# Optimization experiments

Measured on AMD Instinct MI355X. Metric: run time of the kernel, lower is better.

## Reference

```python
import jax, jax.numpy as jnp
import numpy as np

K = 3
P = 14
INV_SQRT2 = 0.7071067811865476  # db1 (Haar) filter coefficient
EPS = 1e-4


def _pool(x):
    # adaptive_avg_pool2d to (P, P); H, W divisible by P -> uniform mean pooling
    N, C, H, W = x.shape
    return x.reshape(N, C, P, H // P, P, W // P).mean(axis=(3, 5))


def setup_inputs() -> dict:
    key = jax.random.key(0)
    ks = jax.random.split(key, 8)
    N, C, H, W = 64, 3, 224, 224
    D, Cin = 540, 30  # D_clip=D_hidden=540, n_bands*3 = 30
    return {
        "frames": jax.random.normal(ks[0], (N, C, H, W), jnp.float32),
        "t_clip": jax.random.normal(ks[1], (N, D, P, P), jnp.float32),
        "w1": jax.random.normal(ks[2], (D, Cin), jnp.float32) * 0.05,
        "b1": jnp.zeros((D,), jnp.float32),
        "w2": jax.random.normal(ks[3], (D, D), jnp.float32) * 0.05,
        "b2": jnp.zeros((D,), jnp.float32),
        "wg": jax.random.normal(ks[4], (D, 2 * D, 3, 3), jnp.float32) * 0.05,
        "bg": jnp.zeros((D,), jnp.float32),
    }


def reference(frames, t_clip, w1, b1, w2, b2, wg, bg):
    # Batched Haar SWT2 (a trous, periodic), levels 1..K, fully vectorized over
    # (N, C) -- replaces the per-frame/per-channel pywt.swt2 CPU loop.
    a = frames
    bands = []  # per level: HL (cH), LH (cV), HH (cD), each (N, C, H, W)
    for j in range(K):
        d = 2 ** j  # filter dilation at level j+1
        lx = (a + jnp.roll(a, -d, axis=-1)) * INV_SQRT2
        hx = (a - jnp.roll(a, -d, axis=-1)) * INV_SQRT2
        cA = (lx + jnp.roll(lx, -d, axis=-2)) * INV_SQRT2
        cH = (lx - jnp.roll(lx, -d, axis=-2)) * INV_SQRT2
        cV = (hx + jnp.roll(hx, -d, axis=-2)) * INV_SQRT2
        cD = (hx - jnp.roll(hx, -d, axis=-2)) * INV_SQRT2
        bands += [cH, cV, cD]
        a = cA
    # per-(frame, channel) 99th-percentile normalization + pool to (P, P)
    pooled = []
    for b in bands:
        s = jnp.quantile(jnp.abs(b), 0.99, axis=(-2, -1), keepdims=True)
        pooled.append(_pool(b / (s + EPS)))
    # LL band (level K approximation): mean-center then quantile-scale
    mu = a.mean(axis=(-2, -1), keepdims=True)
    s = jnp.quantile(jnp.abs(a - mu), 0.99, axis=(-2, -1), keepdims=True)
    pooled.append(_pool((a - mu) / (s + EPS)))
    e_pix = jnp.concatenate(pooled, axis=1)  # (N, 30, P, P)

    # 1x1 conv -> relu -> 1x1 conv -> tanh
    h = jax.nn.relu(jnp.einsum("ncpq,dc->ndpq", e_pix, w1) + b1[None, :, None, None])
    m = jnp.tanh(jnp.einsum("ncpq,dc->ndpq", h, w2) + b2[None, :, None, None])

    # gated fusion with CLIP patch tokens
    gi = jnp.concatenate([t_clip, m], axis=1)  # (N, 2*D, P, P)
    g = jax.lax.conv_general_dilated(
        gi, wg, (1, 1), "SAME", dimension_numbers=("NCHW", "OIHW", "NCHW")
    ) + bg[None, :, None, None]
    gamma = jax.nn.sigmoid(g)
    return t_clip + gamma * m
```

## Files before the change

kernel.cpp:

```cpp
#include <hip/hip_runtime.h>

typedef unsigned short u16;
typedef unsigned int u32;
typedef __bf16 bf16x8 __attribute__((ext_vector_type(8)));
typedef float f32x4 __attribute__((ext_vector_type(4)));

constexpr int NB = 64, CH3 = 3;
constexpr int PLANES = NB * CH3;
constexpr int PPIX = 224 * 224;
constexpr int PP = 196;
constexpr int NPX = NB * PP;
constexpr int K2 = 576;
constexpr int CIPAD = 1088;
constexpr int KCONV = 9 * CIPAD;
constexpr int BINS = 256;
constexpr int BIN0 = 896;
constexpr int RANK1 = 49674;
constexpr int RANK2 = 49675;

constexpr size_t OFF_HIST = 0;
constexpr size_t SZ_HIST  = (size_t)10 * PLANES * BINS * 4;
constexpr size_t OFF_SUMS = OFF_HIST + SZ_HIST;
constexpr size_t OFF_INVS = OFF_SUMS + 768;
constexpr size_t OFF_BSUM = OFF_INVS + 7680;
constexpr size_t SZ_BSUM  = (size_t)10 * PLANES * PP * 4;
constexpr size_t OFF_EPIX = OFF_BSUM + SZ_BSUM;
constexpr size_t OFF_HBF  = OFF_EPIX + (size_t)NPX * 32 * 4;
constexpr size_t OFF_GIT  = OFF_HBF + (size_t)NPX * K2 * 2;
constexpr size_t SZ_GIT   = (size_t)NB * 256 * CIPAD * 2;
constexpr size_t OFF_WGB  = OFF_GIT + SZ_GIT;
constexpr size_t OFF_W2B  = OFF_WGB + (size_t)640 * KCONV * 2;
constexpr size_t OFF_MARR = OFF_W2B + (size_t)640 * K2 * 2;

__device__ __forceinline__ u16 f2bf(float x) {
  union { float f; u32 u; } c; c.f = x;
  u32 r = c.u + 0x7FFFu + ((c.u >> 16) & 1u);
  return (u16)(r >> 16);
}

__device__ __forceinline__ float wred64(float v) {
  v += __shfl_down(v, 32, 64); v += __shfl_down(v, 16, 64);
  v += __shfl_down(v, 8, 64);  v += __shfl_down(v, 4, 64);
  v += __shfl_down(v, 2, 64);  v += __shfl_down(v, 1, 64);
  return v;
}

__device__ __forceinline__ float gred16(float v) {
  v += __shfl_down(v, 8, 16); v += __shfl_down(v, 4, 16);
  v += __shfl_down(v, 2, 16); v += __shfl_down(v, 1, 16);
  return v;
}

__device__ __forceinline__ int hbin(float v) {
  int b = (int)(__float_as_uint(fabsf(v)) >> 20) - BIN0;
  return min(max(b, 0), BINS - 1);
}

__device__ __forceinline__ void cp16(const void* g, void* l) {
  __builtin_amdgcn_global_load_lds((const __attribute__((address_space(1))) u32*)g,
                                   (__attribute__((address_space(3))) u32*)l, 16, 0, 0);
}

__device__ __forceinline__ float fast_tanh(float x) {
  return 1.f - 2.f / (1.f + __expf(2.f * x));
}
__device__ __forceinline__ float fast_sigmoid(float x) {
  return 1.f / (1.f + __expf(-x));
}

#define BAR_MEM() asm volatile("s_barrier" ::: "memory")

constexpr int RSTRIDE = 10 * 128 + 8;
__global__ __launch_bounds__(256) void swt_fused_kernel(const float* __restrict__ frames,
    float* __restrict__ sums, int* __restrict__ hist, float* __restrict__ bsum)
{
  __shared__ float a1[22 * 224];
  __shared__ float a2[20 * 224];
  __shared__ u32 lh[8 * RSTRIDE];
  __shared__ float csum[14 * 10];
  __shared__ float wsum[4];
  const int t = threadIdx.x;
  const int rb = blockIdx.x, plane = blockIdx.y;
  const float* Pp = frames + (size_t)plane * PPIX;

  for (int i = t; i < 8 * RSTRIDE; i += 256) lh[i] = 0;
  __syncthreads();

  u32* lhr = &lh[(t & 7) * RSTRIDE];
  const int cell0 = (t >> 4) * 10;
  float ps = 0.f;

  if (t < 224) {
    int c2 = t + 1; if (c2 >= 224) c2 -= 224;
    float sH = 0.f, sV = 0.f, sD = 0.f;
    int gr0 = rb * 16; if (gr0 >= 224) gr0 -= 224;
    float q00 = Pp[gr0 * 224 + t], q01 = Pp[gr0 * 224 + c2];
    for (int r = 0; r < 22; ++r) {
      int gr1 = rb * 16 + r + 1; if (gr1 >= 224) gr1 -= 224;
      float p10 = Pp[gr1 * 224 + t], p11 = Pp[gr1 * 224 + c2];
      float sa = q00 + q01, sb = p10 + p11, da = q00 - q01, db = p10 - p11;
      a1[r * 224 + t] = (sa + sb) * 0.5f;
      if (r < 16) {
        float cH = (sa - sb) * 0.5f, cV = (da + db) * 0.5f, cD = (da - db) * 0.5f;
        int bH = hbin(cH), bV = hbin(cV), bD = hbin(cD);
        atomicAdd(&lhr[0 * 128 + (bH >> 1)], 1u << ((bH & 1) * 16));
        atomicAdd(&lhr[1 * 128 + (bV >> 1)], 1u << ((bV & 1) * 16));
        atomicAdd(&lhr[2 * 128 + (bD >> 1)], 1u << ((bD & 1) * 16));
        sH += cH; sV += cV; sD += cD;
        ps += q00;
      }
      q00 = p10; q01 = p11;
    }
    sH = gred16(sH); sV = gred16(sV); sD = gred16(sD);
    if ((t & 15) == 0) { csum[cell0 + 0] = sH; csum[cell0 + 1] = sV; csum[cell0 + 2] = sD; }
  }
  ps = wred64(ps);
  if ((t & 63) == 0) wsum[t >> 6] = ps;
  __syncthreads();
  if (t == 0) atomicAdd(&sums[plane], wsum[0] + wsum[1] + wsum[2] + wsum[3]);

  if (t < 224) {
    int c2 = t + 2; if (c2 >= 224) c2 -= 224;
    float sH = 0.f, sV = 0.f, sD = 0.f;
    for (int r = 0; r < 20; ++r) {
      float p00 = a1[r * 224 + t], p01 = a1[r * 224 + c2];
      float p10 = a1[(r + 2) * 224 + t], p11 = a1[(r + 2) * 224 + c2];
      float sa = p00 + p01, sb = p10 + p11, da = p00 - p01, db = p10 - p11;
      a2[r * 224 + t] = (sa + sb) * 0.5f;
      if (r < 16) {
        float cH = (sa - sb) * 0.5f, cV = (da + db) * 0.5f, cD = (da - db) * 0.5f;
        int bH = hbin(cH), bV = hbin(cV), bD = hbin(cD);
        atomicAdd(&lhr[3 * 128 + (bH >> 1)], 1u << ((bH & 1) * 16));
        atomicAdd(&lhr[4 * 128 + (bV >> 1)], 1u << ((bV & 1) * 16));
        atomicAdd(&lhr[5 * 128 + (bD >> 1)], 1u << ((bD & 1) * 16));
        sH += cH; sV += cV; sD += cD;
      }
    }
    sH = gred16(sH); sV = gred16(sV); sD = gred16(sD);
    if ((t & 15) == 0) { csum[cell0 + 3] = sH; csum[cell0 + 4] = sV; csum[cell0 + 5] = sD; }
  }
  __syncthreads();

  if (t < 224) {
    int c2 = t + 4; if (c2 >= 224) c2 -= 224;
    float sH = 0.f, sV = 0.f, sD = 0.f, sA = 0.f;
    for (int r = 0; r < 16; ++r) {
      float p00 = a2[r * 224 + t], p01 = a2[r * 224 + c2];
      float p10 = a2[(r + 4) * 224 + t], p11 = a2[(r + 4) * 224 + c2];
      float sa = p00 + p01, sb = p10 + p11, da = p00 - p01, db = p10 - p11;
      float cA = (sa + sb) * 0.5f;
      float cH = (sa - sb) * 0.5f, cV = (da + db) * 0.5f, cD = (da - db) * 0.5f;
      int bH = hbin(cH), bV = hbin(cV), bD = hbin(cD), bA = hbin(cA);
      atomicAdd(&lhr[6 * 128 + (bH >> 1)], 1u << ((bH & 1) * 16));
      atomicAdd(&lhr[7 * 128 + (bV >> 1)], 1u << ((bV & 1) * 16));
      atomicAdd(&lhr[8 * 128 + (bD >> 1)], 1u << ((bD & 1) * 16));
      atomicAdd(&lhr[9 * 128 + (bA >> 1)], 1u << ((bA & 1) * 16));
      sH += cH; sV += cV; sD += cD; sA += cA;
    }
    sH = gred16(sH); sV = gred16(sV); sD = gred16(sD); sA = gred16(sA);
    if ((t & 15) == 0) {
      csum[cell0 + 6] = sH; csum[cell0 + 7] = sV; csum[cell0 + 8] = sD; csum[cell0 + 9] = sA;
    }
  }
  __syncthreads();

  for (int i = t; i < 10 * 256; i += 256) {
    int bg = i >> 8, b = i & 255;
    u32 acc = 0;
#pragma unroll
    for (int rp = 0; rp < 8; ++rp)
      acc += (lh[rp * RSTRIDE + bg * 128 + (b >> 1)] >> ((b & 1) * 16)) & 0xFFFFu;
    if (acc) atomicAdd(&hist[((size_t)bg * PLANES + plane) * BINS + b], (int)acc);
  }
  if (t < 140) {
    int cell = t / 10, bg = t - cell * 10;
    bsum[((size_t)bg * PLANES + plane) * PP + rb * 14 + cell] = csum[cell * 10 + bg];
  }
}

__global__ __launch_bounds__(256) void quant_kernel(const int* __restrict__ hist,
    float* __restrict__ invs)
{
  const int g = blockIdx.x;
  __shared__ int cum[BINS];
  __shared__ float vv[2];
  const int t = threadIdx.x;
  const int c = hist[(size_t)g * BINS + t];
  cum[t] = c;
  __syncthreads();
  for (int off = 1; off < BINS; off <<= 1) {
    int y = (t >= off) ? cum[t - off] : 0;
    __syncthreads();
    cum[t] += y;
    __syncthreads();
  }
  int inc = cum[t], prev = inc - c;
#pragma unroll
  for (int k = 0; k < 2; ++k) {
    int rank = k ? RANK2 : RANK1;
    if (prev < rank && rank <= inc) {
      float lo = __uint_as_float((u32)(t + BIN0) << 20);
      float hi = __uint_as_float((u32)(t + BIN0 + 1) << 20);
      float fr = ((float)(rank - prev) - 0.5f) / (float)c;
      fr = fminf(fmaxf(fr, 0.f), 1.f);
      vv[k] = lo + (hi - lo) * fr;
    }
  }
  __syncthreads();
  if (t == 0) {
    float s = 0.75f * vv[0] + 0.25f * vv[1];
    invs[g] = 1.f / (s + 1e-4f);
  }
}

__global__ __launch_bounds__(256) void pack_all_kernel(const float* __restrict__ wg,
    const float* __restrict__ w2, const float* __restrict__ tclip,
    u16* __restrict__ wgb, u16* __restrict__ w2b, u16* __restrict__ git)
{
  __shared__ float sh[9720];
  const int bid = blockIdx.x;
  const int t = threadIdx.x;
  if (bid < 640) {
    const int oc = bid;
    if (oc < 540) {
      for (int i = t; i < 9720; i += 256) sh[i] = wg[(size_t)oc * 9720 + i];
    }
    __syncthreads();
    for (int j = t; j < KCONV; j += 256) {
      int kc = j >> 6, i = j & 63;
      int cib = kc / 9, tap = kc - cib * 9;
      int ci = cib * 64 + i;
      float v = (oc < 540 && ci < 1080) ? sh[ci * 9 + tap] : 0.f;
      wgb[(size_t)oc * KCONV + j] = f2bf(v);
    }
  } else if (bid < 2080) {
    int tid = (bid - 640) * 256 + t;
    int oc = tid / K2, cc = tid - oc * K2;
    float v = (oc < 540 && cc < 540) ? w2[oc * 540 + cc] : 0.f;
    w2b[tid] = f2bf(v);
  } else if (bid < 4169) {
    constexpr int CPB = 136;
    constexpr int CPN = 60 * CPB + 196;
    int tid = (bid - 2080) * 256 + t;
    if (tid >= NB * CPN) return;
    int n = tid / CPN, rem = tid - n * CPN;
    int y, x, c;
    if (rem < 60 * CPB) {
      int bi = rem / CPB; c = rem - bi * CPB;
      if (bi < 16) { y = 0; x = bi; }
      else if (bi < 32) { y = 15; x = bi - 16; }
      else { int i = bi - 32; y = 1 + (i >> 1); x = (i & 1) * 15; }
    } else {
      int q = rem - 60 * CPB;
      y = 1 + q / 14; x = 1 + q % 14; c = 135;
    }
    f32x4 z = (f32x4){0.f, 0.f, 0.f, 0.f};
    *reinterpret_cast<f32x4*>(&git[((size_t)(n * 256 + y * 16 + x)) * CIPAD + c * 8]) = z;
  } else {
    int local = bid - 4169;
    int n = local / 36, rem = local - n * 36;
    int ct = rem >> 2, qt = rem & 3;
    const int tr = t >> 6, tc = t & 63;
#pragma unroll 4
    for (int i = 0; i < 16; ++i) {
      int ci = ct * 64 + i * 4 + tr, q = qt * 64 + tc;
      float v = (ci < 540 && q < 196) ? tclip[((size_t)n * 540 + ci) * 196 + q] : 0.f;
      sh[(i * 4 + tr) * 65 + tc] = v;
    }
    __syncthreads();
#pragma unroll 4
    for (int i = 0; i < 16; ++i) {
      int q = qt * 64 + i * 4 + tr, ci = ct * 64 + tc;
      if (q < 196 && ci < 540) {
        int y = q / 14, x = q - y * 14;
        git[(((size_t)n * 16 + 1 + y) * 16 + 1 + x) * CIPAD + ci] = f2bf(sh[tc * 65 + i * 4 + tr]);
      }
    }
  }
}

__global__ __launch_bounds__(256) void gemm1_kernel(const float* __restrict__ bsum,
    const float* __restrict__ sums, const float* __restrict__ invs,
    const float* __restrict__ w1, const float* __restrict__ b1, u16* __restrict__ hbf)
{
  __shared__ float es[64][33];
  __shared__ float w1s[128][33];
  const int t = threadIdx.x;
  const int px0 = blockIdx.x * 64, oc0 = blockIdx.y * 128;
  for (int i = t; i < 64 * 32; i += 256) {
    int r = i >> 5, cc = i & 31;
    int px = px0 + r, n = px / PP, q = px - n * PP;
    float val = 0.f;
    if (cc < 27) {
      int bg = cc / 3, c = cc - bg * 3;
      int plane = n * 3 + c;
      val = bsum[((size_t)bg * PLANES + plane) * PP + q] * (1.f / 256.f) * invs[bg * PLANES + plane];
    } else if (cc < 30) {
      int c = cc - 27, plane = n * 3 + c;
      float mu = sums[plane] * (8.f / 50176.f);
      val = (bsum[((size_t)9 * PLANES + plane) * PP + q] * (1.f / 256.f) - mu) * invs[9 * PLANES + plane];
    }
    es[r][cc] = val;
  }
  for (int i = t; i < 128 * 32; i += 256) {
    int r = i >> 5, cc = i & 31; int oc = oc0 + r;
    w1s[r][cc] = (oc < 540 && cc < 30) ? w1[oc * 30 + cc] : 0.f;
  }
  __syncthreads();
  const int ocl = t & 31, pxl = (t >> 5) * 8;
  float acc[4][8];
#pragma unroll
  for (int i = 0; i < 4; ++i)
#pragma unroll
    for (int j = 0; j < 8; ++j) acc[i][j] = 0.f;
  for (int k = 0; k < 30; ++k) {
    float wv[4], ev[8];
#pragma unroll
    for (int i = 0; i < 4; ++i) wv[i] = w1s[ocl + 32 * i][k];
#pragma unroll
    for (int j = 0; j < 8; ++j) ev[j] = es[pxl + j][k];
#pragma unroll
    for (int i = 0; i < 4; ++i)
#pragma unroll
      for (int j = 0; j < 8; ++j) acc[i][j] += wv[i] * ev[j];
  }
#pragma unroll
  for (int i = 0; i < 4; ++i) {
    int oc = oc0 + ocl + 32 * i;
    if (oc >= 576) continue;
    float bv = (oc < 540) ? b1[oc] : 0.f;
#pragma unroll
    for (int j = 0; j < 8; ++j) {
      int px = px0 + pxl + j;
      float v = (oc < 540) ? fmaxf(acc[i][j] + bv, 0.f) : 0.f;
      hbf[(size_t)px * K2 + oc] = f2bf(v);
    }
  }
}

template <int MODE>
__global__ __launch_bounds__(256) void mfma_gemm_kernel(
    const u16* __restrict__ A, const u16* __restrict__ Bm,
    const float* __restrict__ bias,
    float* __restrict__ marr, u16* __restrict__ git,
    const float* __restrict__ tclip, float* __restrict__ outp)
{
  constexpr int KCPB = (MODE == 1) ? 153 : 9;
  constexpr int BSTRIDE = (MODE == 1) ? KCONV : K2;
  __shared__ u16 smem[32768];
  const int t = threadIdx.x;
  const int lane = t & 63, wave = t >> 6;
  const int wm = wave & 1, wn = wave >> 1;

  int px0, oc0;
  if constexpr (MODE == 1) {
    int orig = blockIdx.x;
    int xcd = orig & 7, off = orig >> 3;
    constexpr int q = 61, r = 2;
    int wg = (xcd < r ? xcd * (q + 1) : r * (q + 1) + (xcd - r) * q) + off;
    int bx = wg / 5, by = wg - bx * 5;
    px0 = bx * 128; oc0 = by * 128;
  } else {
    px0 = blockIdx.x * 128; oc0 = blockIdx.y * 128;
  }

  const u16* aSrc[4];
  const u16* bSrc[4];
  int dstOff[4];
#pragma unroll
  for (int r = 0; r < 4; ++r) {
    int slot = r * 256 + t;
    int row = slot >> 3;
    int gs = ((slot ^ row) & 7) << 3;
    if constexpr (MODE == 0) {
      aSrc[r] = A + (size_t)(px0 + row) * K2 + gs;
    } else {
      int px = px0 + row;
      int n = px / 196, q2 = px - n * 196;
      int y = q2 / 14, x = q2 - y * 14;
      aSrc[r] = A + (size_t)((n * 16 + y) * 16 + x) * CIPAD + gs;
    }
    bSrc[r] = Bm + (size_t)(oc0 + row) * BSTRIDE + gs;
    dstOff[r] = (r * 256 + wave * 64) * 8;
  }

  auto stage = [&](int kcg, int buf) {
    int boff = kcg * 64;
    int aoff;
    if constexpr (MODE == 1) {
      int cib = kcg / 9, tap = kcg - cib * 9;
      int ky = tap / 3, kx = tap - ky * 3;
      aoff = (ky * 16 + kx) * CIPAD + cib * 64;
    } else aoff = boff;
    u16* As = smem + buf * 16384;
    u16* Bs = As + 8192;
#pragma unroll
    for (int r = 0; r < 4; ++r) cp16(aSrc[r] + aoff, As + dstOff[r]);
#pragma unroll
    for (int r = 0; r < 4; ++r) cp16(bSrc[r] + boff, Bs + dstOff[r]);
  };

  const int tx = lane & 15, quad = lane >> 4, l7 = lane & 7;
  int rowA[4], rowB[4];
#pragma unroll
  for (int i = 0; i < 4; ++i) {
    rowA[i] = (wm * 64 + i * 16 + tx) * 64;
    rowB[i] = (wn * 64 + i * 16 + tx) * 64;
  }

  f32x4 acc[4][4];
#pragma unroll
  for (int i = 0; i < 4; ++i)
#pragma unroll
    for (int j = 0; j < 4; ++j) acc[i][j] = (f32x4){0.f, 0.f, 0.f, 0.f};

  stage(0, 0);
  stage(1, 1);
  int cur = 0;
  for (int kc = 0; kc < KCPB; ++kc) {
    if (kc + 1 < KCPB) { asm volatile("s_waitcnt vmcnt(8)" ::: "memory"); }
    else               { asm volatile("s_waitcnt vmcnt(0)" ::: "memory"); }
    BAR_MEM();
    const u16* As = smem + cur * 16384;
    const u16* Bs = As + 8192;
#pragma unroll
    for (int ks = 0; ks < 2; ++ks) {
      int goff = (((ks * 4 + quad) ^ l7) << 3);
      bf16x8 af[4], bfr[4];
#pragma unroll
      for (int i = 0; i < 4; ++i) af[i] = *reinterpret_cast<const bf16x8*>(As + rowA[i] + goff);
#pragma unroll
      for (int i = 0; i < 4; ++i) bfr[i] = *reinterpret_cast<const bf16x8*>(Bs + rowB[i] + goff);
      __builtin_amdgcn_s_setprio(1);
#pragma unroll
      for (int i = 0; i < 4; ++i)
#pragma unroll
        for (int j = 0; j < 4; ++j)
          acc[i][j] = __builtin_amdgcn_mfma_f32_16x16x32_bf16(af[i], bfr[j], acc[i][j], 0, 0, 0);
      __builtin_amdgcn_s_setprio(0);
    }
    BAR_MEM();
    if (kc + 2 < KCPB) stage(kc + 2, cur);
    cur ^= 1;
  }

#pragma unroll
  for (int j = 0; j < 4; ++j) {
    int oc = oc0 + wn * 64 + j * 16 + tx;
    if (oc >= 540) continue;
    float bv = bias[oc];
#pragma unroll
    for (int i = 0; i < 4; ++i) {
      f32x4 v = acc[i][j];
      int px = px0 + wm * 64 + i * 16 + quad * 4;
      int n = px / 196, q2 = px - n * 196;
      size_t idx = ((size_t)(n * 540 + oc)) * 196 + q2;
      if constexpr (MODE == 0) {
#pragma unroll
        for (int r = 0; r < 4; ++r) {
          float val = fast_tanh(v[r] + bv);
          marr[idx + r] = val;
          int qq = q2 + r;
          int y = qq / 14, x = qq - y * 14;
          git[((n * 16 + 1 + y) * 16 + 1 + x) * CIPAD + 540 + oc] = f2bf(val);
        }
      } else {
        f32x4 mv = *reinterpret_cast<const f32x4*>(marr + idx);
        f32x4 tv = *reinterpret_cast<const f32x4*>(tclip + idx);
        f32x4 res;
#pragma unroll
        for (int r = 0; r < 4; ++r) {
          res[r] = tv[r] + mv[r] * fast_sigmoid(v[r] + bv);
        }
        *reinterpret_cast<f32x4*>(outp + idx) = res;
      }
    }
  }
}

extern "C" void kernel_launch(void* const* d_in, const int* in_sizes, int n_in,
                              void* d_out, int out_size, void* d_ws, size_t ws_size,
                              hipStream_t stream)
{
  const float* frames = (const float*)d_in[0];
  const float* t_clip = (const float*)d_in[1];
  const float* w1 = (const float*)d_in[2];
  const float* b1 = (const float*)d_in[3];
  const float* w2 = (const float*)d_in[4];
  const float* b2 = (const float*)d_in[5];
  const float* wg = (const float*)d_in[6];
  const float* bg = (const float*)d_in[7];
  float* out = (float*)d_out;
  char* ws = (char*)d_ws;

  int* HIST = (int*)(ws + OFF_HIST);
  float* SUMS = (float*)(ws + OFF_SUMS);
  float* INVS = (float*)(ws + OFF_INVS);
  float* BSUM = (float*)(ws + OFF_BSUM);
  u16* HBF = (u16*)(ws + OFF_HBF);
  u16* GIT = (u16*)(ws + OFF_GIT);
  u16* WGB = (u16*)(ws + OFF_WGB);
  u16* W2B = (u16*)(ws + OFF_W2B);
  float* MARR = (float*)(ws + OFF_MARR);

  hipMemsetAsync(ws + OFF_HIST, 0, SZ_HIST + 768, stream);

  pack_all_kernel<<<6473, 256, 0, stream>>>(wg, w2, t_clip, WGB, W2B, GIT);

  swt_fused_kernel<<<dim3(14, PLANES), 256, 0, stream>>>(frames, SUMS, HIST, BSUM);
  quant_kernel<<<1920, 256, 0, stream>>>(HIST, INVS);

  gemm1_kernel<<<dim3(196, 5), 256, 0, stream>>>(BSUM, SUMS, INVS, w1, b1, HBF);
  mfma_gemm_kernel<0><<<dim3(98, 5), 256, 0, stream>>>(HBF, W2B, b2, MARR, GIT, nullptr, nullptr);
  mfma_gemm_kernel<1><<<490, 256, 0, stream>>>(GIT, WGB, bg, MARR, nullptr, t_clip, out);
}
```

Before: 494.9 us.

## Merge SWT histogram pass into pack kernel and drop global atomics and memset

The SWT/histogram kernel and the weight/activation pack kernel become one launch, with block-index ranges picking the role, so the two independent phases run concurrently. Global atomic histogram and sum accumulation is replaced by per-row-block partial histograms and partial sums written without atomics. The quant and gemm1 kernels now reduce those 14 partials themselves. This removes the memset and one launch, at the cost of a larger shared-memory footprint per block for the pack roles and extra partial-buffer traffic.

Measured after the change: 488.7 us. About the same (-1.2%).

```diff
diff --git a/kernel.cpp b/kernel.cpp
--- a/kernel.cpp
+++ b/kernel.cpp
@@ -18,19 +18,19 @@
 constexpr int RANK1 = 49674;
 constexpr int RANK2 = 49675;
 
-constexpr size_t OFF_HIST = 0;
-constexpr size_t SZ_HIST  = (size_t)10 * PLANES * BINS * 4;
-constexpr size_t OFF_SUMS = OFF_HIST + SZ_HIST;
-constexpr size_t OFF_INVS = OFF_SUMS + 768;
-constexpr size_t OFF_BSUM = OFF_INVS + 7680;
+constexpr size_t OFF_BSUM = 2 * 1024 * 1024;
 constexpr size_t SZ_BSUM  = (size_t)10 * PLANES * PP * 4;
-constexpr size_t OFF_EPIX = OFF_BSUM + SZ_BSUM;
-constexpr size_t OFF_HBF  = OFF_EPIX + (size_t)NPX * 32 * 4;
+constexpr size_t OFF_INVS = OFF_BSUM + SZ_BSUM;
+constexpr size_t OFF_HBF  = OFF_INVS + 8192;
 constexpr size_t OFF_GIT  = OFF_HBF + (size_t)NPX * K2 * 2;
 constexpr size_t SZ_GIT   = (size_t)NB * 256 * CIPAD * 2;
 constexpr size_t OFF_WGB  = OFF_GIT + SZ_GIT;
 constexpr size_t OFF_W2B  = OFF_WGB + (size_t)640 * KCONV * 2;
 constexpr size_t OFF_MARR = OFF_W2B + (size_t)640 * K2 * 2;
+constexpr size_t SZ_MARR  = (size_t)NPX * 540 * 4;
+constexpr size_t OFF_HISTP = OFF_MARR + SZ_MARR;
+constexpr size_t SZ_HISTP  = (size_t)PLANES * 14 * 2560 * 4;
+constexpr size_t OFF_PSUM  = OFF_HISTP + SZ_HISTP;
 
 __device__ __forceinline__ u16 f2bf(float x) {
   union { float f; u32 u; } c; c.f = x;
@@ -71,177 +71,143 @@
 #define BAR_MEM() asm volatile("s_barrier" ::: "memory")
 
 constexpr int RSTRIDE = 10 * 128 + 8;
-__global__ __launch_bounds__(256) void swt_fused_kernel(const float* __restrict__ frames,
-    float* __restrict__ sums, int* __restrict__ hist, float* __restrict__ bsum)
-{
-  __shared__ float a1[22 * 224];
-  __shared__ float a2[20 * 224];
-  __shared__ u32 lh[8 * RSTRIDE];
-  __shared__ float csum[14 * 10];
-  __shared__ float wsum[4];
-  const int t = threadIdx.x;
-  const int rb = blockIdx.x, plane = blockIdx.y;
-  const float* Pp = frames + (size_t)plane * PPIX;
-
-  for (int i = t; i < 8 * RSTRIDE; i += 256) lh[i] = 0;
-  __syncthreads();
-
-  u32* lhr = &lh[(t & 7) * RSTRIDE];
-  const int cell0 = (t >> 4) * 10;
-  float ps = 0.f;
-
-  if (t < 224) {
-    int c2 = t + 1; if (c2 >= 224) c2 -= 224;
-    float sH = 0.f, sV = 0.f, sD = 0.f;
-    int gr0 = rb * 16; if (gr0 >= 224) gr0 -= 224;
-    float q00 = Pp[gr0 * 224 + t], q01 = Pp[gr0 * 224 + c2];
-    for (int r = 0; r < 22; ++r) {
-      int gr1 = rb * 16 + r + 1; if (gr1 >= 224) gr1 -= 224;
-      float p10 = Pp[gr1 * 224 + t], p11 = Pp[gr1 * 224 + c2];
-      float sa = q00 + q01, sb = p10 + p11, da = q00 - q01, db = p10 - p11;
-      a1[r * 224 + t] = (sa + sb) * 0.5f;
-      if (r < 16) {
-        float cH = (sa - sb) * 0.5f, cV = (da + db) * 0.5f, cD = (da - db) * 0.5f;
-        int bH = hbin(cH), bV = hbin(cV), bD = hbin(cD);
-        atomicAdd(&lhr[0 * 128 + (bH >> 1)], 1u << ((bH & 1) * 16));
-        atomicAdd(&lhr[1 * 128 + (bV >> 1)], 1u << ((bV & 1) * 16));
-        atomicAdd(&lhr[2 * 128 + (bD >> 1)], 1u << ((bD & 1) * 16));
-        sH += cH; sV += cV; sD += cD;
-        ps += q00;
-      }
-      q00 = p10; q01 = p11;
-    }
-    sH = gred16(sH); sV = gred16(sV); sD = gred16(sD);
-    if ((t & 15) == 0) { csum[cell0 + 0] = sH; csum[cell0 + 1] = sV; csum[cell0 + 2] = sD; }
-  }
-  ps = wred64(ps);
-  if ((t & 63) == 0) wsum[t >> 6] = ps;
-  __syncthreads();
-  if (t == 0) atomicAdd(&sums[plane], wsum[0] + wsum[1] + wsum[2] + wsum[3]);
-
-  if (t < 224) {
-    int c2 = t + 2; if (c2 >= 224) c2 -= 224;
-    float sH = 0.f, sV = 0.f, sD = 0.f;
-    for (int r = 0; r < 20; ++r) {
-      float p00 = a1[r * 224 + t], p01 = a1[r * 224 + c2];
-      float p10 = a1[(r + 2) * 224 + t], p11 = a1[(r + 2) * 224 + c2];
-      float sa = p00 + p01, sb = p10 + p11, da = p00 - p01, db = p10 - p11;
-      a2[r * 224 + t] = (sa + sb) * 0.5f;
-      if (r < 16) {
-        float cH = (sa - sb) * 0.5f, cV = (da + db) * 0.5f, cD = (da - db) * 0.5f;
-        int bH = hbin(cH), bV = hbin(cV), bD = hbin(cD);
-        atomicAdd(&lhr[3 * 128 + (bH >> 1)], 1u << ((bH & 1) * 16));
-        atomicAdd(&lhr[4 * 128 + (bV >> 1)], 1u << ((bV & 1) * 16));
-        atomicAdd(&lhr[5 * 128 + (bD >> 1)], 1u << ((bD & 1) * 16));
-        sH += cH; sV += cV; sD += cD;
-      }
-    }
-    sH = gred16(sH); sV = gred16(sV); sD = gred16(sD);
-    if ((t & 15) == 0) { csum[cell0 + 3] = sH; csum[cell0 + 4] = sV; csum[cell0 + 5] = sD; }
-  }
-  __syncthreads();
-
-  if (t < 224) {
-    int c2 = t + 4; if (c2 >= 224) c2 -= 224;
-    float sH = 0.f, sV = 0.f, sD = 0.f, sA = 0.f;
-    for (int r = 0; r < 16; ++r) {
-      float p00 = a2[r * 224 + t], p01 = a2[r * 224 + c2];
-      float p10 = a2[(r + 4) * 224 + t], p11 = a2[(r + 4) * 224 + c2];
-      float sa = p00 + p01, sb = p10 + p11, da = p00 - p01, db = p10 - p11;
-      float cA = (sa + sb) * 0.5f;
-      float cH = (sa - sb) * 0.5f, cV = (da + db) * 0.5f, cD = (da - db) * 0.5f;
-      int bH = hbin(cH), bV = hbin(cV), bD = hbin(cD), bA = hbin(cA);
-      atomicAdd(&lhr[6 * 128 + (bH >> 1)], 1u << ((bH & 1) * 16));
-      atomicAdd(&lhr[7 * 128 + (bV >> 1)], 1u << ((bV & 1) * 16));
-      atomicAdd(&lhr[8 * 128 + (bD >> 1)], 1u << ((bD & 1) * 16));
-      atomicAdd(&lhr[9 * 128 + (bA >> 1)], 1u << ((bA & 1) * 16));
-      sH += cH; sV += cV; sD += cD; sA += cA;
-    }
-    sH = gred16(sH); sV = gred16(sV); sD = gred16(sD); sA = gred16(sA);
-    if ((t & 15) == 0) {
-      csum[cell0 + 6] = sH; csum[cell0 + 7] = sV; csum[cell0 + 8] = sD; csum[cell0 + 9] = sA;
-    }
-  }
-  __syncthreads();
-
-  for (int i = t; i < 10 * 256; i += 256) {
-    int bg = i >> 8, b = i & 255;
-    u32 acc = 0;
-#pragma unroll
-    for (int rp = 0; rp < 8; ++rp)
-      acc += (lh[rp * RSTRIDE + bg * 128 + (b >> 1)] >> ((b & 1) * 16)) & 0xFFFFu;
-    if (acc) atomicAdd(&hist[((size_t)bg * PLANES + plane) * BINS + b], (int)acc);
-  }
-  if (t < 140) {
-    int cell = t / 10, bg = t - cell * 10;
-    bsum[((size_t)bg * PLANES + plane) * PP + rb * 14 + cell] = csum[cell * 10 + bg];
-  }
-}
-
-__global__ __launch_bounds__(256) void quant_kernel(const int* __restrict__ hist,
-    float* __restrict__ invs)
-{
-  const int g = blockIdx.x;
-  __shared__ int cum[BINS];
-  __shared__ float vv[2];
-  const int t = threadIdx.x;
-  const int c = hist[(size_t)g * BINS + t];
-  cum[t] = c;
-  __syncthreads();
-  for (int off = 1; off < BINS; off <<= 1) {
-    int y = (t >= off) ? cum[t - off] : 0;
-    __syncthreads();
-    cum[t] += y;
-    __syncthreads();
-  }
-  int inc = cum[t], prev = inc - c;
-#pragma unroll
-  for (int k = 0; k < 2; ++k) {
-    int rank = k ? RANK2 : RANK1;
-    if (prev < rank && rank <= inc) {
-      float lo = __uint_as_float((u32)(t + BIN0) << 20);
-      float hi = __uint_as_float((u32)(t + BIN0 + 1) << 20);
-      float fr = ((float)(rank - prev) - 0.5f) / (float)c;
-      fr = fminf(fmaxf(fr, 0.f), 1.f);
-      vv[k] = lo + (hi - lo) * fr;
-    }
-  }
-  __syncthreads();
-  if (t == 0) {
-    float s = 0.75f * vv[0] + 0.25f * vv[1];
-    invs[g] = 1.f / (s + 1e-4f);
-  }
-}
-
-__global__ __launch_bounds__(256) void pack_all_kernel(const float* __restrict__ wg,
-    const float* __restrict__ w2, const float* __restrict__ tclip,
+constexpr int SWT_BLOCKS = 14 * PLANES;
+
+__global__ __launch_bounds__(256) void prep_kernel(const float* __restrict__ frames,
+    const float* __restrict__ wg, const float* __restrict__ w2,
+    const float* __restrict__ tclip,
+    float* __restrict__ psum, int* __restrict__ histp, float* __restrict__ bsum,
     u16* __restrict__ wgb, u16* __restrict__ w2b, u16* __restrict__ git)
 {
-  __shared__ float sh[9720];
+  __shared__ float shf[19856];
   const int bid = blockIdx.x;
   const int t = threadIdx.x;
-  if (bid < 640) {
-    const int oc = bid;
+
+  if (bid < SWT_BLOCKS) {
+    float* a1 = shf;
+    float* a2 = shf + 4928;
+    u32* lh = (u32*)(shf + 9408);
+    float* csum = shf + 19712;
+    float* wsum = shf + 19852;
+    const int rb = bid % 14, plane = bid / 14;
+    const float* Pp = frames + (size_t)plane * PPIX;
+
+    for (int i = t; i < 8 * RSTRIDE; i += 256) lh[i] = 0;
+    __syncthreads();
+
+    u32* lhr = &lh[(t & 7) * RSTRIDE];
+    const int cell0 = (t >> 4) * 10;
+    float ps = 0.f;
+
+    if (t < 224) {
+      int c2 = t + 1; if (c2 >= 224) c2 -= 224;
+      float sH = 0.f, sV = 0.f, sD = 0.f;
+      int gr0 = rb * 16; if (gr0 >= 224) gr0 -= 224;
+      float q00 = Pp[gr0 * 224 + t], q01 = Pp[gr0 * 224 + c2];
+      for (int r = 0; r < 22; ++r) {
+        int gr1 = rb * 16 + r + 1; if (gr1 >= 224) gr1 -= 224;
+        float p10 = Pp[gr1 * 224 + t], p11 = Pp[gr1 * 224 + c2];
+        float sa = q00 + q01, sb = p10 + p11, da = q00 - q01, db = p10 - p11;
+        a1[r * 224 + t] = (sa + sb) * 0.5f;
+        if (r < 16) {
+          float cH = (sa - sb) * 0.5f, cV = (da + db) * 0.5f, cD = (da - db) * 0.5f;
+          int bH = hbin(cH), bV = hbin(cV), bD = hbin(cD);
+          atomicAdd(&lhr[0 * 128 + (bH >> 1)], 1u << ((bH & 1) * 16));
+          atomicAdd(&lhr[1 * 128 + (bV >> 1)], 1u << ((bV & 1) * 16));
+          atomicAdd(&lhr[2 * 128 + (bD >> 1)], 1u << ((bD & 1) * 16));
+          sH += cH; sV += cV; sD += cD;
+          ps += q00;
+        }
+        q00 = p10; q01 = p11;
+      }
+      sH = gred16(sH); sV = gred16(sV); sD = gred16(sD);
+      if ((t & 15) == 0) { csum[cell0 + 0] = sH; csum[cell0 + 1] = sV; csum[cell0 + 2] = sD; }
+    }
+    ps = wred64(ps);
+    if ((t & 63) == 0) wsum[t >> 6] = ps;
+    __syncthreads();
+    if (t == 0) psum[plane * 14 + rb] = wsum[0] + wsum[1] + wsum[2] + wsum[3];
+
+    if (t < 224) {
+      int c2 = t + 2; if (c2 >= 224) c2 -= 224;
+      float sH = 0.f, sV = 0.f, sD = 0.f;
+      for (int r = 0; r < 20; ++r) {
+        float p00 = a1[r * 224 + t], p01 = a1[r * 224 + c2];
+        float p10 = a1[(r + 2) * 224 + t], p11 = a1[(r + 2) * 224 + c2];
+        float sa = p00 + p01, sb = p10 + p11, da = p00 - p01, db = p10 - p11;
+        a2[r * 224 + t] = (sa + sb) * 0.5f;
+        if (r < 16) {
+          float cH = (sa - sb) * 0.5f, cV = (da + db) * 0.5f, cD = (da - db) * 0.5f;
+          int bH = hbin(cH), bV = hbin(cV), bD = hbin(cD);
+          atomicAdd(&lhr[3 * 128 + (bH >> 1)], 1u << ((bH & 1) * 16));
+          atomicAdd(&lhr[4 * 128 + (bV >> 1)], 1u << ((bV & 1) * 16));
+          atomicAdd(&lhr[5 * 128 + (bD >> 1)], 1u << ((bD & 1) * 16));
+          sH += cH; sV += cV; sD += cD;
+        }
+      }
+      sH = gred16(sH); sV = gred16(sV); sD = gred16(sD);
+      if ((t & 15) == 0) { csum[cell0 + 3] = sH; csum[cell0 + 4] = sV; csum[cell0 + 5] = sD; }
+    }
+    __syncthreads();
+
+    if (t < 224) {
+      int c2 = t + 4; if (c2 >= 224) c2 -= 224;
+      float sH = 0.f, sV = 0.f, sD = 0.f, sA = 0.f;
+      for (int r = 0; r < 16; ++r) {
+        float p00 = a2[r * 224 + t], p01 = a2[r * 224 + c2];
+        float p10 = a2[(r + 4) * 224 + t], p11 = a2[(r + 4) * 224 + c2];
+        float sa = p00 + p01, sb = p10 + p11, da = p00 - p01, db = p10 - p11;
+        float cA = (sa + sb) * 0.5f;
+        float cH = (sa - sb) * 0.5f, cV = (da + db) * 0.5f, cD = (da - db) * 0.5f;
+        int bH = hbin(cH), bV = hbin(cV), bD = hbin(cD), bA = hbin(cA);
+        atomicAdd(&lhr[6 * 128 + (bH >> 1)], 1u << ((bH & 1) * 16));
+        atomicAdd(&lhr[7 * 128 + (bV >> 1)], 1u << ((bV & 1) * 16));
+        atomicAdd(&lhr[8 * 128 + (bD >> 1)], 1u << ((bD & 1) * 16));
+        atomicAdd(&lhr[9 * 128 + (bA >> 1)], 1u << ((bA & 1) * 16));
+        sH += cH; sV += cV; sD += cD; sA += cA;
+      }
+      sH = gred16(sH); sV = gred16(sV); sD = gred16(sD); sA = gred16(sA);
+      if ((t & 15) == 0) {
+        csum[cell0 + 6] = sH; csum[cell0 + 7] = sV; csum[cell0 + 8] = sD; csum[cell0 + 9] = sA;
+      }
+    }
+    __syncthreads();
+
+    int* hp = histp + ((size_t)plane * 14 + rb) * 2560;
+    for (int i = t; i < 2560; i += 256) {
+      int bg = i >> 8, b = i & 255;
+      u32 acc = 0;
+#pragma unroll
+      for (int rp = 0; rp < 8; ++rp)
+        acc += (lh[rp * RSTRIDE + bg * 128 + (b >> 1)] >> ((b & 1) * 16)) & 0xFFFFu;
+      hp[i] = (int)acc;
+    }
+    if (t < 140) {
+      int cell = t / 10, bg = t - cell * 10;
+      bsum[((size_t)bg * PLANES + plane) * PP + rb * 14 + cell] = csum[cell * 10 + bg];
+    }
+  } else if (bid < SWT_BLOCKS + 640) {
+    const int oc = bid - SWT_BLOCKS;
     if (oc < 540) {
-      for (int i = t; i < 9720; i += 256) sh[i] = wg[(size_t)oc * 9720 + i];
+      for (int i = t; i < 9720; i += 256) shf[i] = wg[(size_t)oc * 9720 + i];
     }
     __syncthreads();
     for (int j = t; j < KCONV; j += 256) {
       int kc = j >> 6, i = j & 63;
       int cib = kc / 9, tap = kc - cib * 9;
       int ci = cib * 64 + i;
-      float v = (oc < 540 && ci < 1080) ? sh[ci * 9 + tap] : 0.f;
+      float v = (oc < 540 && ci < 1080) ? shf[ci * 9 + tap] : 0.f;
       wgb[(size_t)oc * KCONV + j] = f2bf(v);
     }
-  } else if (bid < 2080) {
-    int tid = (bid - 640) * 256 + t;
+  } else if (bid < SWT_BLOCKS + 2080) {
+    int tid = (bid - SWT_BLOCKS - 640) * 256 + t;
     int oc = tid / K2, cc = tid - oc * K2;
     float v = (oc < 540 && cc < 540) ? w2[oc * 540 + cc] : 0.f;
     w2b[tid] = f2bf(v);
-  } else if (bid < 4169) {
+  } else if (bid < SWT_BLOCKS + 4169) {
     constexpr int CPB = 136;
     constexpr int CPN = 60 * CPB + 196;
-    int tid = (bid - 2080) * 256 + t;
+    int tid = (bid - SWT_BLOCKS - 2080) * 256 + t;
     if (tid >= NB * CPN) return;
     int n = tid / CPN, rem = tid - n * CPN;
     int y, x, c;
@@ -257,7 +223,7 @@
     f32x4 z = (f32x4){0.f, 0.f, 0.f, 0.f};
     *reinterpret_cast<f32x4*>(&git[((size_t)(n * 256 + y * 16 + x)) * CIPAD + c * 8]) = z;
   } else {
-    int local = bid - 4169;
+    int local = bid - SWT_BLOCKS - 4169;
     int n = local / 36, rem = local - n * 36;
     int ct = rem >> 2, qt = rem & 3;
     const int tr = t >> 6, tc = t & 63;
@@ -265,7 +231,7 @@
     for (int i = 0; i < 16; ++i) {
       int ci = ct * 64 + i * 4 + tr, q = qt * 64 + tc;
       float v = (ci < 540 && q < 196) ? tclip[((size_t)n * 540 + ci) * 196 + q] : 0.f;
-      sh[(i * 4 + tr) * 65 + tc] = v;
+      shf[(i * 4 + tr) * 65 + tc] = v;
     }
     __syncthreads();
 #pragma unroll 4
@@ -273,14 +239,53 @@
       int q = qt * 64 + i * 4 + tr, ci = ct * 64 + tc;
       if (q < 196 && ci < 540) {
         int y = q / 14, x = q - y * 14;
-        git[(((size_t)n * 16 + 1 + y) * 16 + 1 + x) * CIPAD + ci] = f2bf(sh[tc * 65 + i * 4 + tr]);
+        git[(((size_t)n * 16 + 1 + y) * 16 + 1 + x) * CIPAD + ci] = f2bf(shf[tc * 65 + i * 4 + tr]);
       }
     }
   }
 }
 
+__global__ __launch_bounds__(256) void quant_kernel(const int* __restrict__ histp,
+    float* __restrict__ invs)
+{
+  const int g = blockIdx.x;
+  const int bg = g / PLANES, plane = g - bg * PLANES;
+  __shared__ int cum[BINS];
+  __shared__ float vv[2];
+  const int t = threadIdx.x;
+  const int* hp = histp + (size_t)plane * 14 * 2560 + bg * 256;
+  int c = 0;
+#pragma unroll
+  for (int rb = 0; rb < 14; ++rb) c += hp[rb * 2560 + t];
+  cum[t] = c;
+  __syncthreads();
+  for (int off = 1; off < BINS; off <<= 1) {
+    int y = (t >= off) ? cum[t - off] : 0;
+    __syncthreads();
+    cum[t] += y;
+    __syncthreads();
+  }
+  int inc = cum[t], prev = inc - c;
+#pragma unroll
+  for (int k = 0; k < 2; ++k) {
+    int rank = k ? RANK2 : RANK1;
+    if (prev < rank && rank <= inc) {
+      float lo = __uint_as_float((u32)(t + BIN0) << 20);
+      float hi = __uint_as_float((u32)(t + BIN0 + 1) << 20);
+      float fr = ((float)(rank - prev) - 0.5f) / (float)c;
+      fr = fminf(fmaxf(fr, 0.f), 1.f);
+      vv[k] = lo + (hi - lo) * fr;
+    }
+  }
+  __syncthreads();
+  if (t == 0) {
+    float s = 0.75f * vv[0] + 0.25f * vv[1];
+    invs[g] = 1.f / (s + 1e-4f);
+  }
+}
+
 __global__ __launch_bounds__(256) void gemm1_kernel(const float* __restrict__ bsum,
-    const float* __restrict__ sums, const float* __restrict__ invs,
+    const float* __restrict__ psum, const float* __restrict__ invs,
     const float* __restrict__ w1, const float* __restrict__ b1, u16* __restrict__ hbf)
 {
   __shared__ float es[64][33];
@@ -297,7 +302,10 @@
       val = bsum[((size_t)bg * PLANES + plane) * PP + q] * (1.f / 256.f) * invs[bg * PLANES + plane];
     } else if (cc < 30) {
       int c = cc - 27, plane = n * 3 + c;
-      float mu = sums[plane] * (8.f / 50176.f);
+      float s14 = 0.f;
+#pragma unroll
+      for (int rb = 0; rb < 14; ++rb) s14 += psum[plane * 14 + rb];
+      float mu = s14 * (8.f / 50176.f);
       val = (bsum[((size_t)9 * PLANES + plane) * PP + q] * (1.f / 256.f) - mu) * invs[9 * PLANES + plane];
     }
     es[r][cc] = val;
@@ -493,24 +501,22 @@
   float* out = (float*)d_out;
   char* ws = (char*)d_ws;
 
-  int* HIST = (int*)(ws + OFF_HIST);
-  float* SUMS = (float*)(ws + OFF_SUMS);
+  float* BSUM = (float*)(ws + OFF_BSUM);
   float* INVS = (float*)(ws + OFF_INVS);
-  float* BSUM = (float*)(ws + OFF_BSUM);
   u16* HBF = (u16*)(ws + OFF_HBF);
   u16* GIT = (u16*)(ws + OFF_GIT);
   u16* WGB = (u16*)(ws + OFF_WGB);
   u16* W2B = (u16*)(ws + OFF_W2B);
   float* MARR = (float*)(ws + OFF_MARR);
-
-  hipMemsetAsync(ws + OFF_HIST, 0, SZ_HIST + 768, stream);
-
-  pack_all_kernel<<<6473, 256, 0, stream>>>(wg, w2, t_clip, WGB, W2B, GIT);
-
-  swt_fused_kernel<<<dim3(14, PLANES), 256, 0, stream>>>(frames, SUMS, HIST, BSUM);
-  quant_kernel<<<1920, 256, 0, stream>>>(HIST, INVS);
-
-  gemm1_kernel<<<dim3(196, 5), 256, 0, stream>>>(BSUM, SUMS, INVS, w1, b1, HBF);
+  int* HISTP = (int*)(ws + OFF_HISTP);
+  float* PSUM = (float*)(ws + OFF_PSUM);
+
+  prep_kernel<<<SWT_BLOCKS + 6473, 256, 0, stream>>>(
+      frames, wg, w2, t_clip, PSUM, HISTP, BSUM, WGB, W2B, GIT);
+
+  quant_kernel<<<1920, 256, 0, stream>>>(HISTP, INVS);
+
+  gemm1_kernel<<<dim3(196, 5), 256, 0, stream>>>(BSUM, PSUM, INVS, w1, b1, HBF);
   mfma_gemm_kernel<0><<<dim3(98, 5), 256, 0, stream>>>(HBF, W2B, b2, MARR, GIT, nullptr, nullptr);
   mfma_gemm_kernel<1><<<490, 256, 0, stream>>>(GIT, WGB, bg, MARR, nullptr, t_clip, out);
 }
```
